# Kernel optimization log

Measured on AMD Instinct MI355X. Metric: run time of the kernel, lower is better.

The kernel has to match this reference:

```python
import jax, jax.numpy as jnp
import numpy as np

N = 1048576      # total atoms
B = 16384        # molecules (batch_size)
D = 128          # atom_dim
STEPS = 8


def setup_inputs() -> dict:
    key = jax.random.key(0)
    k1, k2, k3 = jax.random.split(key, 3)
    atom_features = jax.random.normal(k1, (N, D), dtype=jnp.float32)
    atom_partition_indices = jnp.sort(
        jax.random.randint(k2, (N,), 0, B, dtype=jnp.int32))
    # glorot_uniform for (2D, 4D) kernel
    limit = np.sqrt(6.0 / (2 * D + 4 * D)).astype(np.float32)
    recurrent_kernel = jax.random.uniform(
        k3, (2 * D, 4 * D), dtype=jnp.float32, minval=-limit, maxval=limit)
    bias = jnp.zeros((4 * D,), dtype=jnp.float32)
    return {
        "atom_features": atom_features,
        "atom_partition_indices": atom_partition_indices,
        "recurrent_kernel": recurrent_kernel,
        "bias": bias,
        "batch_size": B,
    }


def reference(atom_features, atom_partition_indices, recurrent_kernel, bias,
              batch_size):
    idx = atom_partition_indices
    n_seg = batch_size  # == max(idx)+1 here; all segments occupied
    d = atom_features.shape[-1]
    memory_state = jnp.zeros((n_seg, d), dtype=atom_features.dtype)
    carry_state = jnp.zeros((n_seg, d), dtype=atom_features.dtype)
    carry_state_evolved = jnp.zeros((n_seg, 2 * d), dtype=atom_features.dtype)

    for _ in range(STEPS):
        # attention logits per atom: <atom_features, carry[mol]>
        scores = jnp.sum(atom_features * carry_state[idx], axis=1)  # [N]
        # segment softmax (per molecule)
        seg_max = jax.ops.segment_max(scores, idx, num_segments=n_seg)
        e = jnp.exp(scores - seg_max[idx])
        denom = jax.ops.segment_sum(e, idx, num_segments=n_seg)
        coef = e / denom[idx]                                       # [N]
        # attention readout per molecule
        readout = jax.ops.segment_sum(coef[:, None] * atom_features, idx,
                                      num_segments=n_seg)           # [B, D]
        carry_state_evolved = jnp.concatenate([carry_state, readout], axis=1)
        # no-input LSTM cell
        z = carry_state_evolved @ recurrent_kernel + bias            # [B, 4D]
        u, f, c, o = jnp.split(z, 4, axis=1)
        memory_state = (jax.nn.sigmoid(f) * memory_state
                        + jax.nn.sigmoid(u) * jnp.tanh(c))
        carry_state = jax.nn.sigmoid(o) * jnp.tanh(memory_state)
    return carry_state_evolved
```

## Files before the change

kernel.cpp:

```cpp
#include <hip/hip_runtime.h>
#include <stdint.h>

#define NATOMS 1048576
#define BMOL   16384
#define DIM    128
#define STEPS  8

typedef __attribute__((ext_vector_type(8))) short short8;
typedef __attribute__((ext_vector_type(8))) unsigned short ushort8;
typedef __attribute__((ext_vector_type(4))) float floatx4;

__device__ __forceinline__ float bf2f(unsigned short u) {
    unsigned int x = ((unsigned int)u) << 16;
    float f; __builtin_memcpy(&f, &x, 4); return f;
}
__device__ __forceinline__ unsigned short f2bf(float f) {
    unsigned int x; __builtin_memcpy(&x, &f, 4);
    x = x + 0x7FFFu + ((x >> 16) & 1u);
    return (unsigned short)(x >> 16);
}
__device__ __forceinline__ float sigm(float x) { return 1.f / (1.f + __expf(-x)); }
__device__ __forceinline__ float tanh_fast(float x) {
    float ax = fabsf(x);
    float e = __expf(-2.f * ax);
    float t = (1.f - e) / (1.f + e);
    return x < 0.f ? -t : t;
}

__global__ void detect_kernel(const unsigned short* a, int* flag) {
    __shared__ int bad;
    int tid = threadIdx.x;
    if (tid == 0) bad = 0;
    __syncthreads();
    unsigned short u = a[tid];
    int e = (u >> 7) & 0xFF;
    if (e > 0x85) atomicAdd(&bad, 1);
    __syncthreads();
    if (tid == 0) flag[0] = (bad == 0) ? 1 : 0;
}

__global__ void build_offsets_kernel(const int* idx, int* offsets) {
    int b = blockIdx.x * blockDim.x + threadIdx.x;
    if (b > BMOL) return;
    if (b == BMOL) { offsets[BMOL] = NATOMS; return; }
    int lo = 0, hi = NATOMS;
    while (lo < hi) {
        int mid = (lo + hi) >> 1;
        if (idx[mid] < b) lo = mid + 1; else hi = mid;
    }
    offsets[b] = lo;
}

__global__ void conv_wt_kernel(const float* Wf, const unsigned short* Wb,
                               const int* flag, unsigned short* Wt) {
    int t = blockIdx.x * blockDim.x + threadIdx.x;
    if (t >= 512 * 256) return;
    int n = t >> 8, k = t & 255;
    float v = flag[0] ? bf2f(Wb[k * 512 + n]) : Wf[k * 512 + n];
    Wt[n * 256 + k] = f2bf(v);
}

__global__ __launch_bounds__(256) void mean_conv_kernel(
    const unsigned short* atoms_in_bf, const float* atoms_in_f32,
    unsigned short* atoms_ws, int have_conv, const int* flag,
    const int* offsets, unsigned short* cse)
{
    __shared__ float s_part[16][DIM];

    const int b = blockIdx.x, tid = threadIdx.x;
    const int wid = tid >> 6, lane = tid & 63;
    const int isbf = flag[0];
    const int s = offsets[b], n = offsets[b + 1] - s;

    if (isbf) {
        const int li = lane & 15, g = lane >> 4, p = wid * 4 + g;
        float acc[8];
        #pragma unroll
        for (int j = 0; j < 8; j++) acc[j] = 0.f;
        for (int r = wid * 4 + g; r < n; r += 16) {
            ushort8 u = *(const ushort8*)(atoms_in_bf + (size_t)(s + r) * DIM + li * 8);
            #pragma unroll
            for (int j = 0; j < 8; j++) acc[j] += bf2f(u[j]);
        }
        #pragma unroll
        for (int j = 0; j < 8; j++) s_part[p][li * 8 + j] = acc[j];
    } else {
        const int l32 = lane & 31, h = lane >> 5, p = wid * 2 + h;
        float acc[4];
        #pragma unroll
        for (int j = 0; j < 4; j++) acc[j] = 0.f;
        for (int r = wid * 2 + h; r < n; r += 8) {
            float4 v = *(const float4*)(atoms_in_f32 + (size_t)(s + r) * DIM + l32 * 4);
            acc[0] += v.x; acc[1] += v.y; acc[2] += v.z; acc[3] += v.w;
            if (have_conv) {
                ushort4 o;
                o.x = f2bf(v.x); o.y = f2bf(v.y); o.z = f2bf(v.z); o.w = f2bf(v.w);
                *(ushort4*)(atoms_ws + (size_t)(s + r) * DIM + l32 * 4) = o;
            }
        }
        *(float4*)&s_part[p][l32 * 4] = make_float4(acc[0], acc[1], acc[2], acc[3]);
        *(float4*)&s_part[p + 8][l32 * 4] = make_float4(0.f, 0.f, 0.f, 0.f);
    }
    __syncthreads();

    if (tid < DIM) {
        float R = 0.f;
        #pragma unroll
        for (int p = 0; p < 16; p++) R += s_part[p][tid];
        cse[(size_t)b * 256 + DIM + tid] = f2bf(R / (float)n);
    }
}

__global__ __launch_bounds__(256) void attention_kernel(
    const unsigned short* atoms_in_bf, const float* atoms_in_f32,
    const unsigned short* atoms_ws_bf, int have_conv,
    const int* flag, const int* offsets, const float* carry,
    unsigned short* cse, void* outp, int write_out)
{
    __shared__ float s_part[16][DIM];
    __shared__ float s_m[16];
    __shared__ float s_l[16];

    const int b = blockIdx.x, tid = threadIdx.x;
    const int wid = tid >> 6, lane = tid & 63;
    const int isbf = flag[0];
    const unsigned short* abf = isbf ? atoms_in_bf
                                     : (have_conv ? atoms_ws_bf : nullptr);
    const int s = offsets[b], n = offsets[b + 1] - s;
    const float* crow = carry + (size_t)b * DIM;

    if (abf) {
        const int li = lane & 15, g = lane >> 4, p = wid * 4 + g;
        float c[8], acc[8];
        {
            float4 c0 = *(const float4*)(crow + li * 8);
            float4 c1 = *(const float4*)(crow + li * 8 + 4);
            c[0]=c0.x; c[1]=c0.y; c[2]=c0.z; c[3]=c0.w;
            c[4]=c1.x; c[5]=c1.y; c[6]=c1.z; c[7]=c1.w;
        }
        #pragma unroll
        for (int j = 0; j < 8; j++) acc[j] = 0.f;
        float m = -INFINITY, l = 0.f;

        for (int r = wid * 4 + g; r < n; r += 16) {
            ushort8 u = *(const ushort8*)(abf + (size_t)(s + r) * DIM + li * 8);
            float x[8];
            #pragma unroll
            for (int j = 0; j < 8; j++) x[j] = bf2f(u[j]);
            float pd = x[0]*c[0] + x[1]*c[1] + x[2]*c[2] + x[3]*c[3]
                     + x[4]*c[4] + x[5]*c[5] + x[6]*c[6] + x[7]*c[7];
            pd += __shfl_xor(pd, 1, 64);
            pd += __shfl_xor(pd, 2, 64);
            pd += __shfl_xor(pd, 4, 64);
            pd += __shfl_xor(pd, 8, 64);
            if (pd > m) {
                float al = __expf(m - pd);
                l = l * al + 1.f;
                #pragma unroll
                for (int j = 0; j < 8; j++) acc[j] = acc[j] * al + x[j];
                m = pd;
            } else {
                float ex = __expf(pd - m);
                l += ex;
                #pragma unroll
                for (int j = 0; j < 8; j++) acc[j] += ex * x[j];
            }
        }
        #pragma unroll
        for (int j = 0; j < 8; j++) s_part[p][li * 8 + j] = acc[j];
        if (li == 0) { s_m[p] = m; s_l[p] = l; }
    } else {
        const int l32 = lane & 31, h = lane >> 5, p = wid * 2 + h;
        float4 c4 = *(const float4*)(crow + l32 * 4);
        float acc[4];
        #pragma unroll
        for (int j = 0; j < 4; j++) acc[j] = 0.f;
        float m = -INFINITY, l = 0.f;
        for (int r = wid * 2 + h; r < n; r += 8) {
            float4 v = *(const float4*)(atoms_in_f32 + (size_t)(s + r) * DIM + l32 * 4);
            float pd = v.x*c4.x + v.y*c4.y + v.z*c4.z + v.w*c4.w;
            pd += __shfl_xor(pd, 1, 64);
            pd += __shfl_xor(pd, 2, 64);
            pd += __shfl_xor(pd, 4, 64);
            pd += __shfl_xor(pd, 8, 64);
            pd += __shfl_xor(pd, 16, 64);
            if (pd > m) {
                float al = __expf(m - pd);
                l = l * al + 1.f;
                acc[0] = acc[0]*al + v.x; acc[1] = acc[1]*al + v.y;
                acc[2] = acc[2]*al + v.z; acc[3] = acc[3]*al + v.w;
                m = pd;
            } else {
                float ex = __expf(pd - m);
                l += ex;
                acc[0] += ex*v.x; acc[1] += ex*v.y;
                acc[2] += ex*v.z; acc[3] += ex*v.w;
            }
        }
        *(float4*)&s_part[p][l32 * 4] = make_float4(acc[0], acc[1], acc[2], acc[3]);
        *(float4*)&s_part[p + 8][l32 * 4] = make_float4(0.f, 0.f, 0.f, 0.f);
        if (l32 == 0) { s_m[p] = m; s_l[p] = l; s_m[p + 8] = -INFINITY; s_l[p + 8] = 0.f; }
    }
    __syncthreads();

    if (tid < DIM) {
        float M = -INFINITY;
        #pragma unroll
        for (int p = 0; p < 16; p++) M = fmaxf(M, s_m[p]);
        float L = 0.f, R = 0.f;
        #pragma unroll
        for (int p = 0; p < 16; p++) {
            float w = __expf(s_m[p] - M);
            L += w * s_l[p];
            R += w * s_part[p][tid];
        }
        float r = R / L;
        cse[(size_t)b * 256 + DIM + tid] = f2bf(r);
        if (write_out) {
            float cs = crow[tid];
            if (isbf) {
                unsigned short* ob = (unsigned short*)outp;
                ob[(size_t)b * 256 + tid] = f2bf(cs);
                ob[(size_t)b * 256 + DIM + tid] = f2bf(r);
            } else {
                float* of = (float*)outp;
                of[(size_t)b * 256 + tid] = cs;
                of[(size_t)b * 256 + DIM + tid] = r;
            }
        }
    }
}

#define ZSTRIDE 516
__global__ __launch_bounds__(256) void gemm_lstm_kernel(
    const short* cse, const short* Wt, const float* bias_f,
    const unsigned short* bias_b, const int* flag,
    float* memory, float* carry, unsigned short* cse_out)
{
    __shared__ float s_z[32][ZSTRIDE];

    const int tid = threadIdx.x;
    const int wid = tid >> 6, lane = tid & 63;
    const int lm = lane & 15, quad = lane >> 4;
    const int row0 = blockIdx.x * 32;
    const int col0 = wid * 128;

    floatx4 acc[2][8];
    #pragma unroll
    for (int i = 0; i < 2; i++)
        #pragma unroll
        for (int j = 0; j < 8; j++) acc[i][j] = (floatx4){0.f, 0.f, 0.f, 0.f};

    #pragma unroll
    for (int ks = 0; ks < 8; ks++) {
        const int koff = ks * 32 + quad * 8;
        short8 a0 = *(const short8*)(cse + (size_t)(row0 + lm) * 256 + koff);
        short8 a1 = *(const short8*)(cse + (size_t)(row0 + 16 + lm) * 256 + koff);
        #pragma unroll
        for (int nt = 0; nt < 8; nt++) {
            short8 bw = *(const short8*)(Wt + (size_t)(col0 + nt * 16 + lm) * 256 + koff);
            acc[0][nt] = __builtin_amdgcn_mfma_f32_16x16x32_bf16(a0, bw, acc[0][nt], 0, 0, 0);
            acc[1][nt] = __builtin_amdgcn_mfma_f32_16x16x32_bf16(a1, bw, acc[1][nt], 0, 0, 0);
        }
    }

    const int isbf = flag[0];
    #pragma unroll
    for (int mt = 0; mt < 2; mt++) {
        #pragma unroll
        for (int nt = 0; nt < 8; nt++) {
            int col = col0 + nt * 16 + lm;
            float bv = isbf ? bf2f(bias_b[col]) : bias_f[col];
            #pragma unroll
            for (int i = 0; i < 4; i++) {
                int lr = mt * 16 + quad * 4 + i;
                s_z[lr][col] = acc[mt][nt][i] + bv;
            }
        }
    }
    __syncthreads();

    const int d = tid & 127, rh = tid >> 7;
    for (int r = rh; r < 32; r += 2) {
        float u = s_z[r][d];
        float f = s_z[r][128 + d];
        float c = s_z[r][256 + d];
        float o = s_z[r][384 + d];
        size_t gi = (size_t)(row0 + r) * DIM + d;
        float mem = memory[gi];
        float mnew = sigm(f) * mem + sigm(u) * tanh_fast(c);
        memory[gi] = mnew;
        float cs = sigm(o) * tanh_fast(mnew);
        carry[gi] = cs;
        cse_out[(size_t)(row0 + r) * 256 + d] = f2bf(cs);
    }
}

extern "C" void kernel_launch(void* const* d_in, const int* in_sizes, int n_in,
                              void* d_out, int out_size, void* d_ws, size_t ws_size,
                              hipStream_t stream)
{
    const void* atoms_raw = d_in[0];
    const int*  idx       = (const int*)d_in[1];
    const void* W_raw     = d_in[2];
    const void* bias_raw  = d_in[3];

    char* ws = (char*)d_ws;
    size_t off = 0;
    auto alloc = [&](size_t bytes) {
        size_t p = off;
        off = (off + bytes + 255) & ~(size_t)255;
        return p;
    };
    int*            flag    = (int*)(ws + alloc(4));
    int*            offsets = (int*)(ws + alloc((BMOL + 1) * sizeof(int)));
    float*          carry   = (float*)(ws + alloc((size_t)BMOL * DIM * 4));
    float*          memory  = (float*)(ws + alloc((size_t)BMOL * DIM * 4));
    unsigned short* cse     = (unsigned short*)(ws + alloc((size_t)BMOL * 256 * 2));
    unsigned short* Wt      = (unsigned short*)(ws + alloc(512 * 256 * 2));
    size_t conv_off = alloc((size_t)NATOMS * DIM * 2);
    int have_conv = (ws_size >= off) ? 1 : 0;
    unsigned short* atoms_ws = (unsigned short*)(ws + conv_off);

    detect_kernel<<<1, 256, 0, stream>>>((const unsigned short*)atoms_raw, flag);
    build_offsets_kernel<<<(BMOL + 1 + 255) / 256, 256, 0, stream>>>(idx, offsets);
    conv_wt_kernel<<<512, 256, 0, stream>>>((const float*)W_raw,
                                            (const unsigned short*)W_raw, flag, Wt);
    hipMemsetAsync(memory, 0, (size_t)BMOL * DIM * 4, stream);
    hipMemsetAsync(cse, 0, (size_t)BMOL * 256 * 2, stream);

    mean_conv_kernel<<<BMOL, 256, 0, stream>>>(
        (const unsigned short*)atoms_raw, (const float*)atoms_raw,
        atoms_ws, have_conv, flag, offsets, cse);
    gemm_lstm_kernel<<<BMOL / 32, 256, 0, stream>>>(
        (const short*)cse, (const short*)Wt,
        (const float*)bias_raw, (const unsigned short*)bias_raw, flag,
        memory, carry, cse);

    for (int step = 1; step < STEPS; step++) {
        int last = (step == STEPS - 1);
        attention_kernel<<<BMOL, 256, 0, stream>>>(
            (const unsigned short*)atoms_raw, (const float*)atoms_raw,
            atoms_ws, have_conv, flag, offsets, carry, cse, d_out, last);
        if (!last) {
            gemm_lstm_kernel<<<BMOL / 32, 256, 0, stream>>>(
                (const short*)cse, (const short*)Wt,
                (const float*)bias_raw, (const unsigned short*)bias_raw, flag,
                memory, carry, cse);
        }
    }
}
```

Before: 1.364 ms.

## Fuse all recurrent steps into one persistent kernel per 32-molecule block

Replaces the mean, attention and GEMM+LSTM kernel sequence with a single kernel where each block owns 32 molecules. Carry, memory and the concatenated state stay in LDS and registers across all steps, which removes 15 launches and the global round-trips of the per-step state. Each wave now handles 8 molecules serially with 4 atom rows in flight instead of 16 per molecule. The online softmax becomes branchless and partial states are combined with cross-lane shuffles. The risks are lower occupancy from only 512 blocks and the larger LDS footprint, plus less memory-level parallelism per molecule, which can expose latency on the atom reads that dominate the cost.

```diff
diff --git a/kernel.cpp b/kernel.cpp
--- a/kernel.cpp
+++ b/kernel.cpp
@@ -5,6 +5,8 @@
 #define BMOL   16384
 #define DIM    128
 #define STEPS  8
+#define MPB    32
+#define NBLK   (BMOL / MPB)
 
 typedef __attribute__((ext_vector_type(8))) short short8;
 typedef __attribute__((ext_vector_type(8))) unsigned short ushort8;
@@ -60,239 +62,291 @@
     Wt[n * 256 + k] = f2bf(v);
 }
 
-__global__ __launch_bounds__(256) void mean_conv_kernel(
-    const unsigned short* atoms_in_bf, const float* atoms_in_f32,
-    unsigned short* atoms_ws, int have_conv, const int* flag,
-    const int* offsets, unsigned short* cse)
+__global__ __launch_bounds__(256, 2) void fused_kernel(
+    const unsigned short* __restrict__ atoms_bf,
+    const float* __restrict__ atoms_f32,
+    unsigned short* __restrict__ atoms_ws, int have_conv,
+    const int* __restrict__ flag, const int* __restrict__ offsets,
+    const short* __restrict__ Wt,
+    const float* __restrict__ bias_f, const unsigned short* __restrict__ bias_b,
+    void* __restrict__ outp)
 {
-    __shared__ float s_part[16][DIM];
-
-    const int b = blockIdx.x, tid = threadIdx.x;
+    __shared__ unsigned short s_cse[MPB][264];
+    __shared__ float s_carry[MPB][DIM];
+    __shared__ float s_zq[8][516];
+    __shared__ float s_bias[512];
+    __shared__ int   s_off[MPB + 1];
+
+    const int tid = threadIdx.x;
     const int wid = tid >> 6, lane = tid & 63;
+    const int r0 = blockIdx.x * MPB;
     const int isbf = flag[0];
-    const int s = offsets[b], n = offsets[b + 1] - s;
+
+    if (tid <= MPB) s_off[tid] = offsets[r0 + tid];
+    s_bias[tid]       = isbf ? bf2f(bias_b[tid])       : bias_f[tid];
+    s_bias[256 + tid] = isbf ? bf2f(bias_b[256 + tid]) : bias_f[256 + tid];
+
+    #pragma unroll
+    for (int i = 0; i < 16; i++) {
+        int ii = tid + i * 256;
+        int r = ii >> 7, d = ii & 127;
+        s_carry[r][d] = 0.f;
+        s_cse[r][d] = 0;
+    }
+    float mem[16];
+    #pragma unroll
+    for (int i = 0; i < 16; i++) mem[i] = 0.f;
+
+    __syncthreads();
 
     if (isbf) {
-        const int li = lane & 15, g = lane >> 4, p = wid * 4 + g;
-        float acc[8];
-        #pragma unroll
-        for (int j = 0; j < 8; j++) acc[j] = 0.f;
-        for (int r = wid * 4 + g; r < n; r += 16) {
-            ushort8 u = *(const ushort8*)(atoms_in_bf + (size_t)(s + r) * DIM + li * 8);
-            #pragma unroll
-            for (int j = 0; j < 8; j++) acc[j] += bf2f(u[j]);
+        const int li = lane & 15, g = lane >> 4;
+        for (int t = 0; t < 8; t++) {
+            const int m = wid * 8 + t;
+            const int s = s_off[m], n = s_off[m + 1] - s;
+            float acc[8];
+            #pragma unroll
+            for (int j = 0; j < 8; j++) acc[j] = 0.f;
+            for (int r = g; r < n; r += 4) {
+                ushort8 u = *(const ushort8*)(atoms_bf + (size_t)(s + r) * DIM + li * 8);
+                #pragma unroll
+                for (int j = 0; j < 8; j++) acc[j] += bf2f(u[j]);
+            }
+            #pragma unroll
+            for (int j = 0; j < 8; j++) {
+                acc[j] += __shfl_xor(acc[j], 16, 64);
+                acc[j] += __shfl_xor(acc[j], 32, 64);
+            }
+            if (g == 0) {
+                float inv = (n > 0) ? 1.f / (float)n : 0.f;
+                ushort8 o;
+                #pragma unroll
+                for (int j = 0; j < 8; j++) o[j] = f2bf(acc[j] * inv);
+                *(ushort8*)&s_cse[m][DIM + li * 8] = o;
+            }
         }
-        #pragma unroll
-        for (int j = 0; j < 8; j++) s_part[p][li * 8 + j] = acc[j];
     } else {
-        const int l32 = lane & 31, h = lane >> 5, p = wid * 2 + h;
-        float acc[4];
-        #pragma unroll
-        for (int j = 0; j < 4; j++) acc[j] = 0.f;
-        for (int r = wid * 2 + h; r < n; r += 8) {
-            float4 v = *(const float4*)(atoms_in_f32 + (size_t)(s + r) * DIM + l32 * 4);
-            acc[0] += v.x; acc[1] += v.y; acc[2] += v.z; acc[3] += v.w;
-            if (have_conv) {
+        const int l32 = lane & 31, h = lane >> 5;
+        for (int t = 0; t < 8; t++) {
+            const int m = wid * 8 + t;
+            const int s = s_off[m], n = s_off[m + 1] - s;
+            float a0 = 0.f, a1 = 0.f, a2 = 0.f, a3 = 0.f;
+            for (int r = h; r < n; r += 2) {
+                float4 v = *(const float4*)(atoms_f32 + (size_t)(s + r) * DIM + l32 * 4);
+                if (have_conv) {
+                    ushort4 o;
+                    o.x = f2bf(v.x); o.y = f2bf(v.y); o.z = f2bf(v.z); o.w = f2bf(v.w);
+                    *(ushort4*)(atoms_ws + (size_t)(s + r) * DIM + l32 * 4) = o;
+                }
+                a0 += v.x; a1 += v.y; a2 += v.z; a3 += v.w;
+            }
+            a0 += __shfl_xor(a0, 32, 64);
+            a1 += __shfl_xor(a1, 32, 64);
+            a2 += __shfl_xor(a2, 32, 64);
+            a3 += __shfl_xor(a3, 32, 64);
+            if (h == 0) {
+                float inv = (n > 0) ? 1.f / (float)n : 0.f;
                 ushort4 o;
-                o.x = f2bf(v.x); o.y = f2bf(v.y); o.z = f2bf(v.z); o.w = f2bf(v.w);
-                *(ushort4*)(atoms_ws + (size_t)(s + r) * DIM + l32 * 4) = o;
-            }
-        }
-        *(float4*)&s_part[p][l32 * 4] = make_float4(acc[0], acc[1], acc[2], acc[3]);
-        *(float4*)&s_part[p + 8][l32 * 4] = make_float4(0.f, 0.f, 0.f, 0.f);
-    }
-    __syncthreads();
-
-    if (tid < DIM) {
-        float R = 0.f;
-        #pragma unroll
-        for (int p = 0; p < 16; p++) R += s_part[p][tid];
-        cse[(size_t)b * 256 + DIM + tid] = f2bf(R / (float)n);
-    }
-}
-
-__global__ __launch_bounds__(256) void attention_kernel(
-    const unsigned short* atoms_in_bf, const float* atoms_in_f32,
-    const unsigned short* atoms_ws_bf, int have_conv,
-    const int* flag, const int* offsets, const float* carry,
-    unsigned short* cse, void* outp, int write_out)
-{
-    __shared__ float s_part[16][DIM];
-    __shared__ float s_m[16];
-    __shared__ float s_l[16];
-
-    const int b = blockIdx.x, tid = threadIdx.x;
-    const int wid = tid >> 6, lane = tid & 63;
-    const int isbf = flag[0];
-    const unsigned short* abf = isbf ? atoms_in_bf
-                                     : (have_conv ? atoms_ws_bf : nullptr);
-    const int s = offsets[b], n = offsets[b + 1] - s;
-    const float* crow = carry + (size_t)b * DIM;
-
-    if (abf) {
-        const int li = lane & 15, g = lane >> 4, p = wid * 4 + g;
-        float c[8], acc[8];
-        {
-            float4 c0 = *(const float4*)(crow + li * 8);
-            float4 c1 = *(const float4*)(crow + li * 8 + 4);
-            c[0]=c0.x; c[1]=c0.y; c[2]=c0.z; c[3]=c0.w;
-            c[4]=c1.x; c[5]=c1.y; c[6]=c1.z; c[7]=c1.w;
-        }
-        #pragma unroll
-        for (int j = 0; j < 8; j++) acc[j] = 0.f;
-        float m = -INFINITY, l = 0.f;
-
-        for (int r = wid * 4 + g; r < n; r += 16) {
-            ushort8 u = *(const ushort8*)(abf + (size_t)(s + r) * DIM + li * 8);
-            float x[8];
-            #pragma unroll
-            for (int j = 0; j < 8; j++) x[j] = bf2f(u[j]);
-            float pd = x[0]*c[0] + x[1]*c[1] + x[2]*c[2] + x[3]*c[3]
-                     + x[4]*c[4] + x[5]*c[5] + x[6]*c[6] + x[7]*c[7];
-            pd += __shfl_xor(pd, 1, 64);
-            pd += __shfl_xor(pd, 2, 64);
-            pd += __shfl_xor(pd, 4, 64);
-            pd += __shfl_xor(pd, 8, 64);
-            if (pd > m) {
-                float al = __expf(m - pd);
-                l = l * al + 1.f;
-                #pragma unroll
-                for (int j = 0; j < 8; j++) acc[j] = acc[j] * al + x[j];
-                m = pd;
-            } else {
-                float ex = __expf(pd - m);
-                l += ex;
-                #pragma unroll
-                for (int j = 0; j < 8; j++) acc[j] += ex * x[j];
-            }
-        }
-        #pragma unroll
-        for (int j = 0; j < 8; j++) s_part[p][li * 8 + j] = acc[j];
-        if (li == 0) { s_m[p] = m; s_l[p] = l; }
-    } else {
-        const int l32 = lane & 31, h = lane >> 5, p = wid * 2 + h;
-        float4 c4 = *(const float4*)(crow + l32 * 4);
-        float acc[4];
-        #pragma unroll
-        for (int j = 0; j < 4; j++) acc[j] = 0.f;
-        float m = -INFINITY, l = 0.f;
-        for (int r = wid * 2 + h; r < n; r += 8) {
-            float4 v = *(const float4*)(atoms_in_f32 + (size_t)(s + r) * DIM + l32 * 4);
-            float pd = v.x*c4.x + v.y*c4.y + v.z*c4.z + v.w*c4.w;
-            pd += __shfl_xor(pd, 1, 64);
-            pd += __shfl_xor(pd, 2, 64);
-            pd += __shfl_xor(pd, 4, 64);
-            pd += __shfl_xor(pd, 8, 64);
-            pd += __shfl_xor(pd, 16, 64);
-            if (pd > m) {
-                float al = __expf(m - pd);
-                l = l * al + 1.f;
-                acc[0] = acc[0]*al + v.x; acc[1] = acc[1]*al + v.y;
-                acc[2] = acc[2]*al + v.z; acc[3] = acc[3]*al + v.w;
-                m = pd;
-            } else {
-                float ex = __expf(pd - m);
-                l += ex;
-                acc[0] += ex*v.x; acc[1] += ex*v.y;
-                acc[2] += ex*v.z; acc[3] += ex*v.w;
-            }
-        }
-        *(float4*)&s_part[p][l32 * 4] = make_float4(acc[0], acc[1], acc[2], acc[3]);
-        *(float4*)&s_part[p + 8][l32 * 4] = make_float4(0.f, 0.f, 0.f, 0.f);
-        if (l32 == 0) { s_m[p] = m; s_l[p] = l; s_m[p + 8] = -INFINITY; s_l[p + 8] = 0.f; }
-    }
-    __syncthreads();
-
-    if (tid < DIM) {
-        float M = -INFINITY;
-        #pragma unroll
-        for (int p = 0; p < 16; p++) M = fmaxf(M, s_m[p]);
-        float L = 0.f, R = 0.f;
-        #pragma unroll
-        for (int p = 0; p < 16; p++) {
-            float w = __expf(s_m[p] - M);
-            L += w * s_l[p];
-            R += w * s_part[p][tid];
-        }
-        float r = R / L;
-        cse[(size_t)b * 256 + DIM + tid] = f2bf(r);
-        if (write_out) {
-            float cs = crow[tid];
-            if (isbf) {
-                unsigned short* ob = (unsigned short*)outp;
-                ob[(size_t)b * 256 + tid] = f2bf(cs);
-                ob[(size_t)b * 256 + DIM + tid] = f2bf(r);
-            } else {
-                float* of = (float*)outp;
-                of[(size_t)b * 256 + tid] = cs;
-                of[(size_t)b * 256 + DIM + tid] = r;
+                o.x = f2bf(a0 * inv); o.y = f2bf(a1 * inv);
+                o.z = f2bf(a2 * inv); o.w = f2bf(a3 * inv);
+                *(ushort4*)&s_cse[m][DIM + l32 * 4] = o;
             }
         }
     }
-}
-
-#define ZSTRIDE 516
-__global__ __launch_bounds__(256) void gemm_lstm_kernel(
-    const short* cse, const short* Wt, const float* bias_f,
-    const unsigned short* bias_b, const int* flag,
-    float* memory, float* carry, unsigned short* cse_out)
-{
-    __shared__ float s_z[32][ZSTRIDE];
-
-    const int tid = threadIdx.x;
-    const int wid = tid >> 6, lane = tid & 63;
-    const int lm = lane & 15, quad = lane >> 4;
-    const int row0 = blockIdx.x * 32;
-    const int col0 = wid * 128;
-
-    floatx4 acc[2][8];
-    #pragma unroll
-    for (int i = 0; i < 2; i++)
-        #pragma unroll
-        for (int j = 0; j < 8; j++) acc[i][j] = (floatx4){0.f, 0.f, 0.f, 0.f};
-
-    #pragma unroll
-    for (int ks = 0; ks < 8; ks++) {
-        const int koff = ks * 32 + quad * 8;
-        short8 a0 = *(const short8*)(cse + (size_t)(row0 + lm) * 256 + koff);
-        short8 a1 = *(const short8*)(cse + (size_t)(row0 + 16 + lm) * 256 + koff);
-        #pragma unroll
-        for (int nt = 0; nt < 8; nt++) {
-            short8 bw = *(const short8*)(Wt + (size_t)(col0 + nt * 16 + lm) * 256 + koff);
-            acc[0][nt] = __builtin_amdgcn_mfma_f32_16x16x32_bf16(a0, bw, acc[0][nt], 0, 0, 0);
-            acc[1][nt] = __builtin_amdgcn_mfma_f32_16x16x32_bf16(a1, bw, acc[1][nt], 0, 0, 0);
+
+    const unsigned short* abf = isbf ? atoms_bf : (have_conv ? atoms_ws : nullptr);
+
+    for (int it = 0; it < STEPS - 1; it++) {
+        __syncthreads();
+
+        {
+            const int lm = lane & 15, quad = lane >> 4;
+            const int col0 = wid * 128;
+            floatx4 acc[2][8];
+            #pragma unroll
+            for (int i = 0; i < 2; i++)
+                #pragma unroll
+                for (int j = 0; j < 8; j++) acc[i][j] = (floatx4){0.f, 0.f, 0.f, 0.f};
+
+            #pragma unroll
+            for (int ks = 0; ks < 8; ks++) {
+                const int koff = ks * 32 + quad * 8;
+                short8 A0 = *(const short8*)&s_cse[lm][koff];
+                short8 A1 = *(const short8*)&s_cse[16 + lm][koff];
+                #pragma unroll
+                for (int nt = 0; nt < 8; nt++) {
+                    short8 bw = *(const short8*)(Wt + (size_t)(col0 + nt * 16 + lm) * 256 + koff);
+                    acc[0][nt] = __builtin_amdgcn_mfma_f32_16x16x32_bf16(A0, bw, acc[0][nt], 0, 0, 0);
+                    acc[1][nt] = __builtin_amdgcn_mfma_f32_16x16x32_bf16(A1, bw, acc[1][nt], 0, 0, 0);
+                }
+            }
+            const int d = tid & 127, rh = tid >> 7;
+            #pragma unroll
+            for (int qq = 0; qq < 4; qq++) {
+                const int mt = qq >> 1, qh = qq & 1;
+                if ((quad >> 1) == qh) {
+                    #pragma unroll
+                    for (int nt = 0; nt < 8; nt++) {
+                        const int col = col0 + nt * 16 + lm;
+                        const float bv = s_bias[col];
+                        #pragma unroll
+                        for (int i = 0; i < 4; i++)
+                            s_zq[(quad & 1) * 4 + i][col] = acc[mt][nt][i] + bv;
+                    }
+                }
+                __syncthreads();
+                #pragma unroll
+                for (int k = 0; k < 4; k++) {
+                    const int lr = rh + k * 2;
+                    const int r = qq * 8 + lr;
+                    float zu = s_zq[lr][d];
+                    float zf = s_zq[lr][128 + d];
+                    float zc = s_zq[lr][256 + d];
+                    float zo = s_zq[lr][384 + d];
+                    float mv = sigm(zf) * mem[qq * 4 + k] + sigm(zu) * tanh_fast(zc);
+                    mem[qq * 4 + k] = mv;
+                    float cs = sigm(zo) * tanh_fast(mv);
+                    s_carry[r][d] = cs;
+                    s_cse[r][d] = f2bf(cs);
+                }
+                __syncthreads();
+            }
         }
-    }
-
-    const int isbf = flag[0];
-    #pragma unroll
-    for (int mt = 0; mt < 2; mt++) {
-        #pragma unroll
-        for (int nt = 0; nt < 8; nt++) {
-            int col = col0 + nt * 16 + lm;
-            float bv = isbf ? bf2f(bias_b[col]) : bias_f[col];
-            #pragma unroll
-            for (int i = 0; i < 4; i++) {
-                int lr = mt * 16 + quad * 4 + i;
-                s_z[lr][col] = acc[mt][nt][i] + bv;
+
+        const int last = (it == STEPS - 2);
+        if (abf) {
+            const int li = lane & 15, g = lane >> 4;
+            for (int t = 0; t < 8; t++) {
+                const int m = wid * 8 + t;
+                const int s = s_off[m], n = s_off[m + 1] - s;
+                float c[8];
+                {
+                    float4 c0 = *(const float4*)&s_carry[m][li * 8];
+                    float4 c1 = *(const float4*)&s_carry[m][li * 8 + 4];
+                    c[0] = c0.x; c[1] = c0.y; c[2] = c0.z; c[3] = c0.w;
+                    c[4] = c1.x; c[5] = c1.y; c[6] = c1.z; c[7] = c1.w;
+                }
+                float acc[8];
+                #pragma unroll
+                for (int j = 0; j < 8; j++) acc[j] = 0.f;
+                float mx = -INFINITY, l = 0.f;
+                for (int r = g; r < n; r += 4) {
+                    ushort8 u = *(const ushort8*)(abf + (size_t)(s + r) * DIM + li * 8);
+                    float x[8];
+                    #pragma unroll
+                    for (int j = 0; j < 8; j++) x[j] = bf2f(u[j]);
+                    float pd = x[0]*c[0] + x[1]*c[1] + x[2]*c[2] + x[3]*c[3]
+                             + x[4]*c[4] + x[5]*c[5] + x[6]*c[6] + x[7]*c[7];
+                    pd += __shfl_xor(pd, 1, 64);
+                    pd += __shfl_xor(pd, 2, 64);
+                    pd += __shfl_xor(pd, 4, 64);
+                    pd += __shfl_xor(pd, 8, 64);
+                    float nm = fmaxf(mx, pd);
+                    float sa = __expf(mx - nm);
+                    float ex = __expf(pd - nm);
+                    l = l * sa + ex;
+                    #pragma unroll
+                    for (int j = 0; j < 8; j++) acc[j] = acc[j] * sa + ex * x[j];
+                    mx = nm;
+                }
+                for (int off = 16; off < 64; off <<= 1) {
+                    float m2 = __shfl_xor(mx, off, 64);
+                    float l2 = __shfl_xor(l, off, 64);
+                    float nm = fmaxf(mx, m2);
+                    float sa = (mx == nm) ? 1.f : __expf(mx - nm);
+                    float sb = (m2 == nm) ? 1.f : __expf(m2 - nm);
+                    l = l * sa + l2 * sb;
+                    #pragma unroll
+                    for (int j = 0; j < 8; j++) {
+                        float a2 = __shfl_xor(acc[j], off, 64);
+                        acc[j] = acc[j] * sa + a2 * sb;
+                    }
+                    mx = nm;
+                }
+                float invl = (l > 0.f) ? 1.f / l : 0.f;
+                if (g == 0) {
+                    if (!last) {
+                        ushort8 o;
+                        #pragma unroll
+                        for (int j = 0; j < 8; j++) o[j] = f2bf(acc[j] * invl);
+                        *(ushort8*)&s_cse[m][DIM + li * 8] = o;
+                    } else {
+                        const size_t gm = (size_t)(r0 + m) * 256;
+                        if (isbf) {
+                            unsigned short* ob = (unsigned short*)outp;
+                            ushort8 oc, orr;
+                            #pragma unroll
+                            for (int j = 0; j < 8; j++) {
+                                oc[j]  = f2bf(c[j]);
+                                orr[j] = f2bf(acc[j] * invl);
+                            }
+                            *(ushort8*)(ob + gm + li * 8) = oc;
+                            *(ushort8*)(ob + gm + DIM + li * 8) = orr;
+                        } else {
+                            float* of = (float*)outp;
+                            *(float4*)(of + gm + li * 8)     = make_float4(c[0], c[1], c[2], c[3]);
+                            *(float4*)(of + gm + li * 8 + 4) = make_float4(c[4], c[5], c[6], c[7]);
+                            *(float4*)(of + gm + DIM + li * 8) =
+                                make_float4(acc[0]*invl, acc[1]*invl, acc[2]*invl, acc[3]*invl);
+                            *(float4*)(of + gm + DIM + li * 8 + 4) =
+                                make_float4(acc[4]*invl, acc[5]*invl, acc[6]*invl, acc[7]*invl);
+                        }
+                    }
+                }
+            }
+        } else {
+            const int l32 = lane & 31, h = lane >> 5;
+            for (int t = 0; t < 8; t++) {
+                const int m = wid * 8 + t;
+                const int s = s_off[m], n = s_off[m + 1] - s;
+                float4 c4 = *(const float4*)&s_carry[m][l32 * 4];
+                float a0 = 0.f, a1 = 0.f, a2 = 0.f, a3 = 0.f;
+                float mx = -INFINITY, l = 0.f;
+                for (int r = h; r < n; r += 2) {
+                    float4 v = *(const float4*)(atoms_f32 + (size_t)(s + r) * DIM + l32 * 4);
+                    float pd = v.x*c4.x + v.y*c4.y + v.z*c4.z + v.w*c4.w;
+                    pd += __shfl_xor(pd, 1, 64);
+                    pd += __shfl_xor(pd, 2, 64);
+                    pd += __shfl_xor(pd, 4, 64);
+                    pd += __shfl_xor(pd, 8, 64);
+                    pd += __shfl_xor(pd, 16, 64);
+                    float nm = fmaxf(mx, pd);
+                    float sa = __expf(mx - nm);
+                    float ex = __expf(pd - nm);
+                    l = l * sa + ex;
+                    a0 = a0 * sa + ex * v.x; a1 = a1 * sa + ex * v.y;
+                    a2 = a2 * sa + ex * v.z; a3 = a3 * sa + ex * v.w;
+                    mx = nm;
+                }
+                {
+                    float m2 = __shfl_xor(mx, 32, 64);
+                    float l2 = __shfl_xor(l, 32, 64);
+                    float nm = fmaxf(mx, m2);
+                    float sa = (mx == nm) ? 1.f : __expf(mx - nm);
+                    float sb = (m2 == nm) ? 1.f : __expf(m2 - nm);
+                    l = l * sa + l2 * sb;
+                    float b0 = __shfl_xor(a0, 32, 64), b1 = __shfl_xor(a1, 32, 64);
+                    float b2 = __shfl_xor(a2, 32, 64), b3 = __shfl_xor(a3, 32, 64);
+                    a0 = a0 * sa + b0 * sb; a1 = a1 * sa + b1 * sb;
+                    a2 = a2 * sa + b2 * sb; a3 = a3 * sa + b3 * sb;
+                }
+                float invl = (l > 0.f) ? 1.f / l : 0.f;
+                if (h == 0) {
+                    if (!last) {
+                        ushort4 o;
+                        o.x = f2bf(a0 * invl); o.y = f2bf(a1 * invl);
+                        o.z = f2bf(a2 * invl); o.w = f2bf(a3 * invl);
+                        *(ushort4*)&s_cse[m][DIM + l32 * 4] = o;
+                    } else {
+                        float* of = (float*)outp;
+                        const size_t gm = (size_t)(r0 + m) * 256;
+                        *(float4*)(of + gm + l32 * 4) = c4;
+                        *(float4*)(of + gm + DIM + l32 * 4) =
+                            make_float4(a0*invl, a1*invl, a2*invl, a3*invl);
+                    }
+                }
             }
         }
-    }
-    __syncthreads();
-
-    const int d = tid & 127, rh = tid >> 7;
-    for (int r = rh; r < 32; r += 2) {
-        float u = s_z[r][d];
-        float f = s_z[r][128 + d];
-        float c = s_z[r][256 + d];
-        float o = s_z[r][384 + d];
-        size_t gi = (size_t)(row0 + r) * DIM + d;
-        float mem = memory[gi];
-        float mnew = sigm(f) * mem + sigm(u) * tanh_fast(c);
-        memory[gi] = mnew;
-        float cs = sigm(o) * tanh_fast(mnew);
-        carry[gi] = cs;
-        cse_out[(size_t)(row0 + r) * 256 + d] = f2bf(cs);
     }
 }
 
@@ -314,9 +368,6 @@
     };
     int*            flag    = (int*)(ws + alloc(4));
     int*            offsets = (int*)(ws + alloc((BMOL + 1) * sizeof(int)));
-    float*          carry   = (float*)(ws + alloc((size_t)BMOL * DIM * 4));
-    float*          memory  = (float*)(ws + alloc((size_t)BMOL * DIM * 4));
-    unsigned short* cse     = (unsigned short*)(ws + alloc((size_t)BMOL * 256 * 2));
     unsigned short* Wt      = (unsigned short*)(ws + alloc(512 * 256 * 2));
     size_t conv_off = alloc((size_t)NATOMS * DIM * 2);
     int have_conv = (ws_size >= off) ? 1 : 0;
@@ -326,27 +377,8 @@
     build_offsets_kernel<<<(BMOL + 1 + 255) / 256, 256, 0, stream>>>(idx, offsets);
     conv_wt_kernel<<<512, 256, 0, stream>>>((const float*)W_raw,
                                             (const unsigned short*)W_raw, flag, Wt);
-    hipMemsetAsync(memory, 0, (size_t)BMOL * DIM * 4, stream);
-    hipMemsetAsync(cse, 0, (size_t)BMOL * 256 * 2, stream);
-
-    mean_conv_kernel<<<BMOL, 256, 0, stream>>>(
+    fused_kernel<<<NBLK, 256, 0, stream>>>(
         (const unsigned short*)atoms_raw, (const float*)atoms_raw,
-        atoms_ws, have_conv, flag, offsets, cse);
-    gemm_lstm_kernel<<<BMOL / 32, 256, 0, stream>>>(
-        (const short*)cse, (const short*)Wt,
-        (const float*)bias_raw, (const unsigned short*)bias_raw, flag,
-        memory, carry, cse);
-
-    for (int step = 1; step < STEPS; step++) {
-        int last = (step == STEPS - 1);
-        attention_kernel<<<BMOL, 256, 0, stream>>>(
-            (const unsigned short*)atoms_raw, (const float*)atoms_raw,
-            atoms_ws, have_conv, flag, offsets, carry, cse, d_out, last);
-        if (!last) {
-            gemm_lstm_kernel<<<BMOL / 32, 256, 0, stream>>>(
-                (const short*)cse, (const short*)Wt,
-                (const float*)bias_raw, (const unsigned short*)bias_raw, flag,
-                memory, carry, cse);
-        }
-    }
-}
+        atoms_ws, have_conv, flag, offsets, (const short*)Wt,
+        (const float*)bias_raw, (const unsigned short*)bias_raw, d_out);
+}
```

New measurement: 1.812 ms. 1.33x slower.
